# Performance work log

Hardware: AMD Instinct MI355X
Metric: run time of the kernel (lower is better)

The kernel has to match this reference:

```python
import jax, jax.numpy as jnp
import numpy as np

GOP = 4


def conv3x3(x, w, b):
    y = jax.lax.conv_general_dilated(x, w, (1, 1), 'SAME',
                                     dimension_numbers=('NCHW', 'OIHW', 'NCHW'))
    return y + b[None, :, None, None]


def resize_bilinear(x, oh, ow):
    # F.interpolate(mode='bilinear', align_corners=False), no antialias
    N, C, H, W = x.shape
    ys = (jnp.arange(oh, dtype=x.dtype) + 0.5) * (H / oh) - 0.5
    xs = (jnp.arange(ow, dtype=x.dtype) + 0.5) * (W / ow) - 0.5
    y0 = jnp.floor(ys); x0 = jnp.floor(xs)
    ty = (ys - y0)[:, None]; tx = (xs - x0)[None, :]
    y0i = jnp.clip(y0, 0, H - 1).astype(jnp.int32)
    y1i = jnp.clip(y0 + 1, 0, H - 1).astype(jnp.int32)
    x0i = jnp.clip(x0, 0, W - 1).astype(jnp.int32)
    x1i = jnp.clip(x0 + 1, 0, W - 1).astype(jnp.int32)
    r00 = x[:, :, y0i][:, :, :, x0i]; r01 = x[:, :, y0i][:, :, :, x1i]
    r10 = x[:, :, y1i][:, :, :, x0i]; r11 = x[:, :, y1i][:, :, :, x1i]
    top = r00 * (1 - tx) + r01 * tx
    bot = r10 * (1 - tx) + r11 * tx
    return top * (1 - ty) + bot * ty


def deform_sample_1x1(feat, off):
    # torchvision deform_conv2d with 1x1 kernel: bilinear gather at
    # (h + dy, w + dx), zero outside; offset channels are (dy, dx).
    N, C, H, W = feat.shape
    dy, dx = off[:, 0], off[:, 1]                       # [N,H,W]
    gy = jnp.arange(H, dtype=feat.dtype)[:, None] + dy  # [N,H,W]
    gx = jnp.arange(W, dtype=feat.dtype)[None, :] + dx
    y0 = jnp.floor(gy); x0 = jnp.floor(gx)
    ty = (gy - y0)[:, None]; tx = (gx - x0)[:, None]    # [N,1,H,W]

    def corner(yi, xi):
        valid = (yi >= 0) & (yi < H) & (xi >= 0) & (xi < W)
        yc = jnp.clip(yi, 0, H - 1).astype(jnp.int32)
        xc = jnp.clip(xi, 0, W - 1).astype(jnp.int32)
        v = jax.vmap(lambda f, y, x: f[:, y, x])(feat, yc, xc)  # [N,C,H,W]
        return v * valid[:, None].astype(feat.dtype)

    return (corner(y0, x0) * (1 - ty) * (1 - tx)
            + corner(y0, x0 + 1) * (1 - ty) * tx
            + corner(y0 + 1, x0) * ty * (1 - tx)
            + corner(y0 + 1, x0 + 1) * ty * tx)


def setup_inputs() -> dict:
    key = jax.random.key(0)
    ks = jax.random.split(key, 20)
    dim = 256
    f32 = jnp.float32

    def p(k, shape, s=0.05):
        return jax.random.normal(k, shape, dtype=f32) * s

    return {
        'imgs': jax.random.normal(ks[0], (2, 16, 3, 224, 224), dtype=f32),
        'i_features': jax.random.normal(ks[1], (8, dim, 56, 56), dtype=f32),
        'p_motions': jax.random.normal(ks[2], (2, 12, 2, 112, 112), dtype=f32),
        'dw': p(ks[3], (dim, dim)), 'db': p(ks[4], (dim,)),
        'mw1': p(ks[5], (dim, dim, 3, 3)), 'mb1': p(ks[6], (dim,)),
        'mw2': p(ks[7], (dim, dim, 3, 3)), 'mb2': p(ks[8], (dim,)),
        'mw3': p(ks[9], (dim, dim, 3, 3)), 'mb3': p(ks[10], (dim,)),
        'ew1': p(ks[11], (dim, 2, 3, 3)), 'eb1': p(ks[12], (dim,)),
        'ew2': p(ks[13], (dim, dim, 3, 3)), 'eb2': p(ks[14], (dim,)),
        'ew3': p(ks[15], (dim, dim, 3, 3)), 'eb3': p(ks[16], (dim,)),
        'ew4': p(ks[17], (dim, dim, 3, 3)), 'eb4': p(ks[18], (dim,)),
    }


def reference(imgs, i_features, p_motions, dw, db, mw1, mb1, mw2, mb2, mw3, mb3,
              ew1, eb1, ew2, eb2, ew3, eb3, ew4, eb4):
    B = imgs.shape[0]
    num_gop = imgs.shape[1] // GOP
    h, w = i_features.shape[-2], i_features.shape[-1]
    scale = h / imgs.shape[-1]  # static python float
    Tp = p_motions.shape[1]
    k = Tp // num_gop

    # flatten motions over (b t), resize to feature res, rescale magnitudes
    pm = p_motions.reshape(B * Tp, 2, p_motions.shape[-2], p_motions.shape[-1])
    pm = resize_bilinear(pm, h, w) * scale              # [(b n k), 2, h, w]

    emb = jax.nn.relu(conv3x3(pm, ew1, eb1))
    emb = jax.nn.relu(conv3x3(emb, ew2, eb2))
    emb = jax.nn.relu(conv3x3(emb, ew3, eb3))
    emb = jax.nn.relu(conv3x3(emb, ew4, eb4))

    # i_features expanded to one copy per P-frame: (b n) -> (b n k)
    feat = jnp.repeat(i_features, k, axis=0)
    sampled = deform_sample_1x1(feat, pm)
    pf = jnp.einsum('nchw,oc->nohw', sampled, dw) + db[None, :, None, None]

    pf = jax.nn.relu(conv3x3(pf, mw1, mb1))
    pf = jax.nn.relu(conv3x3(pf, mw2, mb2))
    pf = jax.nn.relu(conv3x3(pf, mw3, mb3))
    p2d = pf + emb                                      # [(b n k), c, h, w]

    # adaptive_avg_pool2d(1) + flatten(3)
    pooled = p2d.reshape(B, num_gop, k, -1, h, w).mean(axis=(-2, -1))  # [b,n,k,c]
    return pooled, p2d
```

## Files before the change

### kernel.cpp

```cpp
#include <hip/hip_runtime.h>

#define NPIX 3136
#define NN   24
#define CDIM 256

typedef __attribute__((ext_vector_type(8))) short short8v;
typedef __attribute__((ext_vector_type(4))) float float4v;

typedef __attribute__((address_space(1))) const void gvoid;
typedef __attribute__((address_space(3))) void lvoid;
static __device__ __forceinline__ void async_copy16(const void* g, void* l) {
    __builtin_amdgcn_global_load_lds((gvoid*)g, (lvoid*)l, 16, 0, 0);
}

static __device__ __forceinline__ unsigned short f2b(float f) {
    unsigned int u = __float_as_uint(f);
    u = (u + 0x7FFFu + ((u >> 16) & 1u)) >> 16;
    return (unsigned short)u;
}
static __device__ __forceinline__ float b2f(unsigned short h) {
    return __uint_as_float(((unsigned int)h) << 16);
}

__global__ __launch_bounds__(256) void resize_pm_kernel(
    const float* __restrict__ pmo, float* __restrict__ pm)
{
    int idx = blockIdx.x * 256 + threadIdx.x;
    if (idx >= NN * 2 * NPIX) return;
    int x = idx % 56, y = (idx / 56) % 56, nc = idx / NPIX;
    const float* src = pmo + (size_t)nc * 112 * 112 + (size_t)(2 * y) * 112 + 2 * x;
    pm[idx] = (src[0] + src[1] + src[112] + src[113]) * 0.0625f;
}

__global__ __launch_bounds__(256) void pack_all_kernel(
    const float* __restrict__ s0, const float* __restrict__ s1,
    const float* __restrict__ s2, const float* __restrict__ s3,
    const float* __restrict__ s4, const float* __restrict__ s5,
    const float* __restrict__ sdw, unsigned short* __restrict__ dstbase)
{
    int bx = blockIdx.x;
    if (bx < 6 * 2304) {
        int wi = bx / 2304;
        int d = (bx % 2304) * 256 + threadIdx.x;
        const float* w = (wi == 0) ? s0 : (wi == 1) ? s1 : (wi == 2) ? s2
                       : (wi == 3) ? s3 : (wi == 4) ? s4 : s5;
        int j = d & 7;
        int lane = (d >> 3) & 63;
        int g = (d >> 9) & 3;
        int e = d >> 11;
        int tap = e % 9;
        int f = e / 9;
        int ch = f & 7, cb = f >> 3;
        int co = cb * 64 + g * 16 + (lane & 15);
        int ci = ch * 32 + (lane >> 4) * 8 + j;
        dstbase[(size_t)wi * 589824 + d] = f2b(w[((size_t)co * 256 + ci) * 9 + tap]);
    } else {
        int d = (bx - 6 * 2304) * 256 + threadIdx.x;
        int j = d & 7;
        int lane = (d >> 3) & 63;
        int g = (d >> 9) & 3;
        int ch = (d >> 11) & 7;
        int cb = d >> 14;
        int co = cb * 64 + g * 16 + (lane & 15);
        int ci = ch * 32 + (lane >> 4) * 8 + j;
        dstbase[(size_t)6 * 589824 + d] = f2b(sdw[(size_t)co * 256 + ci]);
    }
}

__global__ __launch_bounds__(256) void ew1_kernel(
    const float* __restrict__ pm, const float* __restrict__ w,
    const float* __restrict__ b, unsigned short* __restrict__ out)
{
    __shared__ float sT[8][18];
    __shared__ float sW1[256 * 19];
    int n = blockIdx.y;
    int pixbase = blockIdx.x * 8;
    int t = threadIdx.x;
    if (t < 144) {
        int p = t / 18, j = t % 18;
        int ci = j / 9, tap = j % 9;
        int pix = pixbase + p;
        int y = pix / 56, x = pix % 56;
        int yy = y + tap / 3 - 1, xx = x + tap % 3 - 1;
        float v = 0.f;
        if ((unsigned)yy < 56u && (unsigned)xx < 56u)
            v = pm[((size_t)n * 2 + ci) * NPIX + yy * 56 + xx];
        sT[p][j] = v;
    }
    for (int idx = t; idx < 4608; idx += 256) {
        int co = idx / 18, j = idx % 18;
        sW1[co * 19 + j] = w[idx];
    }
    __syncthreads();
    int co = t;
    float bias = b[co];
#pragma unroll
    for (int p = 0; p < 8; p++) {
        float acc = bias;
#pragma unroll
        for (int j = 0; j < 18; j++) acc += sT[p][j] * sW1[co * 19 + j];
        acc = fmaxf(acc, 0.f);
        out[((size_t)n * NPIX + pixbase + p) * 256 + co] = f2b(acc);
    }
}

template <int TAPS, bool RELU, bool HASB, bool FUSE>
__global__ __launch_bounds__(256, 2) void conv_mfma(
    const unsigned short* __restrict__ in,
    const unsigned short* __restrict__ wp,
    const float* __restrict__ bias,
    unsigned short* __restrict__ out,
    const unsigned short* __restrict__ emb,
    float* __restrict__ dout)
{
    constexpr int W_ITERS = TAPS * 4;
    constexpr int SIN_SHORTS = (TAPS == 9) ? 10 * 58 * 32 : 448 * 32;

    __shared__ unsigned short sIn[SIN_SHORTS];
    __shared__ unsigned short sW[W_ITERS * 512];

    const int r0 = blockIdx.x * 8;
    if (r0 >= 56) return;
    const int tid = threadIdx.x;
    const int lane = tid & 63;
    const int wv = tid >> 6;
    const int col = lane & 15;
    const int quad = lane >> 4;
    const int cb = blockIdx.y;
    const int n = blockIdx.z;

    const unsigned short* inN = in + (size_t)n * NPIX * 256;
    const unsigned short* wcb = wp + (size_t)cb * 8 * W_ITERS * 512;

    int rowoff[7];
#pragma unroll
    for (int nj = 0; nj < 7; nj++) {
        int pxl = wv * 112 + nj * 16 + col;
        if (TAPS == 9) {
            int yl = pxl / 56;
            rowoff[nj] = yl * 58 + (pxl - yl * 56);
        } else {
            rowoff[nj] = pxl;
        }
    }
    const int qoff = quad * 8;
    const int laneSrc = (lane >> 2) * 256 + (lane & 3) * 8;

    if (TAPS == 9) {
        for (int i = tid * 8; i < SIN_SHORTS; i += 2048)
            *(int4*)(sIn + i) = (int4){0, 0, 0, 0};
    }

    float4v acc[4][7];
#pragma unroll
    for (int mi = 0; mi < 4; mi++)
#pragma unroll
        for (int nj = 0; nj < 7; nj++) acc[mi][nj] = (float4v){0.f, 0.f, 0.f, 0.f};

    for (int ch = 0; ch < 8; ch++) {
        const int c0 = ch * 32;
        __syncthreads();
        const unsigned short* wchunk = wcb + (size_t)ch * W_ITERS * 512;
#pragma unroll
        for (int it = wv; it < W_ITERS; it += 4)
            async_copy16(wchunk + it * 512 + lane * 8, sW + it * 512);
        if (TAPS == 9) {
#pragma unroll
            for (int ry = 0; ry < 10; ry++) {
                int k = (wv - ry) & 3;
                int gy = r0 + ry - 1;
                if ((unsigned)gy < 56u && (k < 3 || lane < 32))
                    async_copy16(inN + (size_t)gy * 14336 + k * 4096 + c0 + laneSrc,
                                 sIn + ry * 1856 + 32 + k * 512);
            }
        } else {
#pragma unroll
            for (int k = 0; k < 7; k++) {
                int it = wv + k * 4;
                async_copy16(inN + (size_t)r0 * 14336 + it * 4096 + c0 + laneSrc,
                             sIn + it * 512);
            }
        }
        __syncthreads();
#pragma unroll
        for (int tap = 0; tap < TAPS; tap++) {
            const int coff = (TAPS == 9) ? ((tap / 3) * 58 + (tap % 3)) * 32 : 0;
            short8v a[4], b[7];
#pragma unroll
            for (int mi = 0; mi < 4; mi++)
                a[mi] = *(const short8v*)(sW + ((tap * 4 + mi) * 64 + lane) * 8);
#pragma unroll
            for (int nj = 0; nj < 7; nj++)
                b[nj] = *(const short8v*)(sIn + rowoff[nj] * 32 + coff + qoff);
#pragma unroll
            for (int mi = 0; mi < 4; mi++)
#pragma unroll
                for (int nj = 0; nj < 7; nj++)
                    acc[mi][nj] = __builtin_amdgcn_mfma_f32_16x16x32_bf16(
                        a[mi], b[nj], acc[mi][nj], 0, 0, 0);
        }
    }

    if (!FUSE) {
        unsigned short* outT = out + ((size_t)n * NPIX + r0 * 56 + wv * 112) * 256 + cb * 64;
#pragma unroll
        for (int mi = 0; mi < 4; mi++) {
            float4v bv = (float4v){0.f, 0.f, 0.f, 0.f};
            if (HASB) bv = *(const float4v*)(bias + cb * 64 + mi * 16 + quad * 4);
#pragma unroll
            for (int nj = 0; nj < 7; nj++) {
                float v0 = acc[mi][nj][0] + bv[0];
                float v1 = acc[mi][nj][1] + bv[1];
                float v2 = acc[mi][nj][2] + bv[2];
                float v3 = acc[mi][nj][3] + bv[3];
                if (RELU) {
                    v0 = fmaxf(v0, 0.f); v1 = fmaxf(v1, 0.f);
                    v2 = fmaxf(v2, 0.f); v3 = fmaxf(v3, 0.f);
                }
                uint2 pk;
                pk.x = (unsigned)f2b(v0) | ((unsigned)f2b(v1) << 16);
                pk.y = (unsigned)f2b(v2) | ((unsigned)f2b(v3) << 16);
                *(uint2*)(outT + ((size_t)(nj * 16 + col)) * 256 + mi * 16 + quad * 4) = pk;
            }
        }
    } else {
        const int pixBase = r0 * 56 + wv * 112;
        float* p2d = dout + 6144 + (size_t)n * CDIM * NPIX;
        float sums[4][4];
#pragma unroll
        for (int mi = 0; mi < 4; mi++)
#pragma unroll
            for (int q = 0; q < 4; q++) sums[mi][q] = 0.f;
#pragma unroll
        for (int mi = 0; mi < 4; mi++) {
            float4v bv = *(const float4v*)(bias + cb * 64 + mi * 16 + quad * 4);
            const int co0 = cb * 64 + mi * 16 + quad * 4;
#pragma unroll
            for (int nj = 0; nj < 7; nj++) {
                int pix = pixBase + nj * 16 + col;
                uint2 e = *(const uint2*)(emb + ((size_t)n * NPIX + pix) * 256 + co0);
                float v0 = fmaxf(acc[mi][nj][0] + bv[0], 0.f) + b2f((unsigned short)(e.x & 0xFFFF));
                float v1 = fmaxf(acc[mi][nj][1] + bv[1], 0.f) + b2f((unsigned short)(e.x >> 16));
                float v2 = fmaxf(acc[mi][nj][2] + bv[2], 0.f) + b2f((unsigned short)(e.y & 0xFFFF));
                float v3 = fmaxf(acc[mi][nj][3] + bv[3], 0.f) + b2f((unsigned short)(e.y >> 16));
                p2d[(size_t)(co0 + 0) * NPIX + pix] = v0;
                p2d[(size_t)(co0 + 1) * NPIX + pix] = v1;
                p2d[(size_t)(co0 + 2) * NPIX + pix] = v2;
                p2d[(size_t)(co0 + 3) * NPIX + pix] = v3;
                sums[mi][0] += v0; sums[mi][1] += v1;
                sums[mi][2] += v2; sums[mi][3] += v3;
            }
        }
#pragma unroll
        for (int mi = 0; mi < 4; mi++)
#pragma unroll
            for (int q = 0; q < 4; q++) {
                float s = sums[mi][q];
                s += __shfl_down(s, 8, 16);
                s += __shfl_down(s, 4, 16);
                s += __shfl_down(s, 2, 16);
                s += __shfl_down(s, 1, 16);
                if (col == 0)
                    atomicAdd(dout + n * CDIM + cb * 64 + mi * 16 + quad * 4 + q,
                              s * (1.f / 3136.f));
            }
    }
}

__global__ __launch_bounds__(256) void transpose_fI(
    const float* __restrict__ feat, unsigned short* __restrict__ dst)
{
    __shared__ float s[64][65];
    int fi = blockIdx.z;
    int p0 = blockIdx.x * 64;
    int c0 = blockIdx.y * 64;
    int t = threadIdx.x;
    int pl = t & 63, cq = t >> 6;
#pragma unroll
    for (int i = 0; i < 16; i++) {
        int c = cq + i * 4;
        s[pl][c] = feat[((size_t)fi * 256 + c0 + c) * NPIX + p0 + pl];
    }
    __syncthreads();
    int cl = t & 63, pq = t >> 6;
#pragma unroll
    for (int i = 0; i < 16; i++) {
        int p = pq + i * 4;
        dst[((size_t)fi * NPIX + p0 + p) * 256 + c0 + cl] = f2b(s[p][cl]);
    }
}

__global__ __launch_bounds__(256) void deform_kernel(
    const unsigned short* __restrict__ Z,
    const float* __restrict__ pm,
    const float* __restrict__ db,
    unsigned short* __restrict__ out)
{
    int n = blockIdx.y;
    int t = threadIdx.x;
    int pix = blockIdx.x * 8 + (t >> 5);
    int g = t & 31;
    int fi = n / 3;
    int y = pix / 56, x = pix % 56;
    float dy = pm[((size_t)n * 2 + 0) * NPIX + pix];
    float dx = pm[((size_t)n * 2 + 1) * NPIX + pix];
    float gy = (float)y + dy, gx = (float)x + dx;
    float y0f = floorf(gy), x0f = floorf(gx);
    float ty = gy - y0f, tx = gx - x0f;
    int y0 = (int)y0f, x0 = (int)x0f, y1 = y0 + 1, x1 = x0 + 1;
    bool vy0 = (unsigned)y0 < 56u, vy1 = (unsigned)y1 < 56u;
    bool vx0 = (unsigned)x0 < 56u, vx1 = (unsigned)x1 < 56u;
    float w00 = (1.f - ty) * (1.f - tx) * (vy0 && vx0 ? 1.f : 0.f);
    float w01 = (1.f - ty) * tx * (vy0 && vx1 ? 1.f : 0.f);
    float w10 = ty * (1.f - tx) * (vy1 && vx0 ? 1.f : 0.f);
    float w11 = ty * tx * (vy1 && vx1 ? 1.f : 0.f);
    int y0c = vy0 ? y0 : 0, y1c = vy1 ? y1 : 0;
    int x0c = vx0 ? x0 : 0, x1c = vx1 ? x1 : 0;
    const unsigned short* Zf = Z + (size_t)fi * NPIX * 256 + g * 8;
    const unsigned short* p00 = Zf + (size_t)(y0c * 56 + x0c) * 256;
    const unsigned short* p01 = Zf + (size_t)(y0c * 56 + x1c) * 256;
    const unsigned short* p10 = Zf + (size_t)(y1c * 56 + x0c) * 256;
    const unsigned short* p11 = Zf + (size_t)(y1c * 56 + x1c) * 256;
    unsigned short r[8];
#pragma unroll
    for (int j = 0; j < 8; j++) {
        float v = b2f(p00[j]) * w00 + b2f(p01[j]) * w01 +
                  b2f(p10[j]) * w10 + b2f(p11[j]) * w11;
        v += db[g * 8 + j];
        r[j] = f2b(v);
    }
    *(int4*)(out + ((size_t)n * NPIX + pix) * 256 + g * 8) = *(int4*)r;
}

extern "C" void kernel_launch(void* const* d_in, const int* in_sizes, int n_in,
                              void* d_out, int out_size, void* d_ws, size_t ws_size,
                              hipStream_t stream)
{
    const float* i_features = (const float*)d_in[1];
    const float* p_motions  = (const float*)d_in[2];
    const float* dw  = (const float*)d_in[3];
    const float* db  = (const float*)d_in[4];
    const float* mw1 = (const float*)d_in[5];
    const float* mb1 = (const float*)d_in[6];
    const float* mw2 = (const float*)d_in[7];
    const float* mb2 = (const float*)d_in[8];
    const float* mw3 = (const float*)d_in[9];
    const float* mb3 = (const float*)d_in[10];
    const float* ew1 = (const float*)d_in[11];
    const float* eb1 = (const float*)d_in[12];
    const float* ew2 = (const float*)d_in[13];
    const float* eb2 = (const float*)d_in[14];
    const float* ew3 = (const float*)d_in[15];
    const float* eb3 = (const float*)d_in[16];
    const float* ew4 = (const float*)d_in[17];
    const float* eb4 = (const float*)d_in[18];
    float* out = (float*)d_out;

    char* p = (char*)d_ws;
    float* pm = (float*)p;            p += 602112;
    unsigned short* wpk = (unsigned short*)p;
    unsigned short* wpE2 = wpk + 0 * 589824;
    unsigned short* wpE3 = wpk + 1 * 589824;
    unsigned short* wpE4 = wpk + 2 * 589824;
    unsigned short* wpM1 = wpk + 3 * 589824;
    unsigned short* wpM2 = wpk + 4 * 589824;
    unsigned short* wpM3 = wpk + 5 * 589824;
    unsigned short* wpDW = wpk + 6 * 589824;
    p += (6 * 589824 + 65536) * 2;
    unsigned short* actA = (unsigned short*)p; p += 38535168;
    unsigned short* actB = (unsigned short*)p; p += 38535168;
    unsigned short* embB = (unsigned short*)p; p += 38535168;

    hipMemsetAsync(out, 0, 6144 * sizeof(float), stream);

    resize_pm_kernel<<<(NN * 2 * NPIX + 255) / 256, 256, 0, stream>>>(p_motions, pm);
    pack_all_kernel<<<6 * 2304 + 256, 256, 0, stream>>>(
        ew2, ew3, ew4, mw1, mw2, mw3, dw, wpk);

    ew1_kernel<<<dim3(392, NN), 256, 0, stream>>>(pm, ew1, eb1, actA);
    dim3 cg24(8, 4, NN), cg8(8, 4, 8);
    conv_mfma<9, true, true, false><<<cg24, 256, 0, stream>>>(actA, wpE2, eb2, actB, nullptr, nullptr);
    conv_mfma<9, true, true, false><<<cg24, 256, 0, stream>>>(actB, wpE3, eb3, actA, nullptr, nullptr);
    conv_mfma<9, true, true, false><<<cg24, 256, 0, stream>>>(actA, wpE4, eb4, embB, nullptr, nullptr);

    transpose_fI<<<dim3(49, 4, 8), 256, 0, stream>>>(i_features, actA);
    conv_mfma<1, false, false, false><<<cg8, 256, 0, stream>>>(actA, wpDW, nullptr, actB, nullptr, nullptr);
    deform_kernel<<<dim3(392, NN), 256, 0, stream>>>(actB, pm, db, actA);

    conv_mfma<9, true, true, false><<<cg24, 256, 0, stream>>>(actA, wpM1, mb1, actB, nullptr, nullptr);
    conv_mfma<9, true, true, false><<<cg24, 256, 0, stream>>>(actB, wpM2, mb2, actA, nullptr, nullptr);
    conv_mfma<9, true, true, true><<<cg24, 256, 0, stream>>>(actA, wpM3, mb3, nullptr, embB, out);
}
```

Measured before the change: 712.1 us.

## Co-launch independent embedding and motion conv layers in one paired grid

Adds a second set of input, weight, bias and output pointers plus a z-split to the MFMA conv kernel. Blocks past the split run the other branch's layer. Embedding convs 3 and 4 now run in the same launch as motion convs 1 and 2, doubling the grid. The aim is to cut wave-quantization tail and launch count on this small per-layer grid. It needs a fourth activation buffer and falls back to the old sequential schedule when the workspace is too small.

```diff
diff --git a/kernel.cpp b/kernel.cpp
--- a/kernel.cpp
+++ b/kernel.cpp
@@ -110,6 +110,11 @@
     const unsigned short* __restrict__ wp,
     const float* __restrict__ bias,
     unsigned short* __restrict__ out,
+    const unsigned short* __restrict__ inB,
+    const unsigned short* __restrict__ wpB,
+    const float* __restrict__ biasB,
+    unsigned short* __restrict__ outB,
+    int zsplit,
     const unsigned short* __restrict__ emb,
     float* __restrict__ dout)
 {
@@ -127,10 +132,19 @@
     const int col = lane & 15;
     const int quad = lane >> 4;
     const int cb = blockIdx.y;
-    const int n = blockIdx.z;
-
-    const unsigned short* inN = in + (size_t)n * NPIX * 256;
-    const unsigned short* wcb = wp + (size_t)cb * 8 * W_ITERS * 512;
+
+    int n = blockIdx.z;
+    const unsigned short* inP = in;
+    const unsigned short* wpP = wp;
+    const float* biasP = bias;
+    unsigned short* outP = out;
+    if (n >= zsplit) {
+        n -= zsplit;
+        inP = inB; wpP = wpB; biasP = biasB; outP = outB;
+    }
+
+    const unsigned short* inN = inP + (size_t)n * NPIX * 256;
+    const unsigned short* wcb = wpP + (size_t)cb * 8 * W_ITERS * 512;
 
     int rowoff[7];
 #pragma unroll
@@ -202,11 +216,11 @@
     }
 
     if (!FUSE) {
-        unsigned short* outT = out + ((size_t)n * NPIX + r0 * 56 + wv * 112) * 256 + cb * 64;
+        unsigned short* outT = outP + ((size_t)n * NPIX + r0 * 56 + wv * 112) * 256 + cb * 64;
 #pragma unroll
         for (int mi = 0; mi < 4; mi++) {
             float4v bv = (float4v){0.f, 0.f, 0.f, 0.f};
-            if (HASB) bv = *(const float4v*)(bias + cb * 64 + mi * 16 + quad * 4);
+            if (HASB) bv = *(const float4v*)(biasP + cb * 64 + mi * 16 + quad * 4);
 #pragma unroll
             for (int nj = 0; nj < 7; nj++) {
                 float v0 = acc[mi][nj][0] + bv[0];
@@ -233,7 +247,7 @@
             for (int q = 0; q < 4; q++) sums[mi][q] = 0.f;
 #pragma unroll
         for (int mi = 0; mi < 4; mi++) {
-            float4v bv = *(const float4v*)(bias + cb * 64 + mi * 16 + quad * 4);
+            float4v bv = *(const float4v*)(biasP + cb * 64 + mi * 16 + quad * 4);
             const int co0 = cb * 64 + mi * 16 + quad * 4;
 #pragma unroll
             for (int nj = 0; nj < 7; nj++) {
@@ -356,8 +370,11 @@
     const float* eb4 = (const float*)d_in[18];
     float* out = (float*)d_out;
 
+    const size_t SZ_PM  = 602112;
+    const size_t SZ_WPK = 7208960;
+    const size_t SZ_ACT = 38535168;
     char* p = (char*)d_ws;
-    float* pm = (float*)p;            p += 602112;
+    float* pm = (float*)p;            p += SZ_PM;
     unsigned short* wpk = (unsigned short*)p;
     unsigned short* wpE2 = wpk + 0 * 589824;
     unsigned short* wpE3 = wpk + 1 * 589824;
@@ -366,10 +383,13 @@
     unsigned short* wpM2 = wpk + 4 * 589824;
     unsigned short* wpM3 = wpk + 5 * 589824;
     unsigned short* wpDW = wpk + 6 * 589824;
-    p += (6 * 589824 + 65536) * 2;
-    unsigned short* actA = (unsigned short*)p; p += 38535168;
-    unsigned short* actB = (unsigned short*)p; p += 38535168;
-    unsigned short* embB = (unsigned short*)p; p += 38535168;
+    p += SZ_WPK;
+    unsigned short* bufA = (unsigned short*)p; p += SZ_ACT;
+    unsigned short* bufB = (unsigned short*)p; p += SZ_ACT;
+    unsigned short* bufC = (unsigned short*)p; p += SZ_ACT;
+    unsigned short* bufD = (unsigned short*)p;
+
+    const bool paired = ws_size >= SZ_PM + SZ_WPK + 4 * SZ_ACT;
 
     hipMemsetAsync(out, 0, 6144 * sizeof(float), stream);
 
@@ -377,17 +397,41 @@
     pack_all_kernel<<<6 * 2304 + 256, 256, 0, stream>>>(
         ew2, ew3, ew4, mw1, mw2, mw3, dw, wpk);
 
-    ew1_kernel<<<dim3(392, NN), 256, 0, stream>>>(pm, ew1, eb1, actA);
-    dim3 cg24(8, 4, NN), cg8(8, 4, 8);
-    conv_mfma<9, true, true, false><<<cg24, 256, 0, stream>>>(actA, wpE2, eb2, actB, nullptr, nullptr);
-    conv_mfma<9, true, true, false><<<cg24, 256, 0, stream>>>(actB, wpE3, eb3, actA, nullptr, nullptr);
-    conv_mfma<9, true, true, false><<<cg24, 256, 0, stream>>>(actA, wpE4, eb4, embB, nullptr, nullptr);
-
-    transpose_fI<<<dim3(49, 4, 8), 256, 0, stream>>>(i_features, actA);
-    conv_mfma<1, false, false, false><<<cg8, 256, 0, stream>>>(actA, wpDW, nullptr, actB, nullptr, nullptr);
-    deform_kernel<<<dim3(392, NN), 256, 0, stream>>>(actB, pm, db, actA);
-
-    conv_mfma<9, true, true, false><<<cg24, 256, 0, stream>>>(actA, wpM1, mb1, actB, nullptr, nullptr);
-    conv_mfma<9, true, true, false><<<cg24, 256, 0, stream>>>(actB, wpM2, mb2, actA, nullptr, nullptr);
-    conv_mfma<9, true, true, true><<<cg24, 256, 0, stream>>>(actA, wpM3, mb3, nullptr, embB, out);
-}
+    dim3 cg24(8, 4, NN), cg48(8, 4, 2 * NN), cg8(8, 4, 8);
+
+    if (paired) {
+        ew1_kernel<<<dim3(392, NN), 256, 0, stream>>>(pm, ew1, eb1, bufA);
+        conv_mfma<9, true, true, false><<<cg24, 256, 0, stream>>>(
+            bufA, wpE2, eb2, bufB,  bufA, wpE2, eb2, bufB, NN, nullptr, nullptr);
+        unsigned short* fI = bufA;
+        unsigned short* Zb = bufA + (size_t)8 * NPIX * 256;
+        transpose_fI<<<dim3(49, 4, 8), 256, 0, stream>>>(i_features, fI);
+        conv_mfma<1, false, false, false><<<cg8, 256, 0, stream>>>(
+            fI, wpDW, nullptr, Zb,  fI, wpDW, nullptr, Zb, NN, nullptr, nullptr);
+        deform_kernel<<<dim3(392, NN), 256, 0, stream>>>(Zb, pm, db, bufC);
+        conv_mfma<9, true, true, false><<<cg48, 256, 0, stream>>>(
+            bufB, wpE3, eb3, bufA,  bufC, wpM1, mb1, bufD, NN, nullptr, nullptr);
+        conv_mfma<9, true, true, false><<<cg48, 256, 0, stream>>>(
+            bufA, wpE4, eb4, bufB,  bufD, wpM2, mb2, bufC, NN, nullptr, nullptr);
+        conv_mfma<9, true, true, true><<<cg24, 256, 0, stream>>>(
+            bufC, wpM3, mb3, nullptr,  bufC, wpM3, mb3, nullptr, NN, bufB, out);
+    } else {
+        ew1_kernel<<<dim3(392, NN), 256, 0, stream>>>(pm, ew1, eb1, bufA);
+        conv_mfma<9, true, true, false><<<cg24, 256, 0, stream>>>(
+            bufA, wpE2, eb2, bufB,  bufA, wpE2, eb2, bufB, NN, nullptr, nullptr);
+        conv_mfma<9, true, true, false><<<cg24, 256, 0, stream>>>(
+            bufB, wpE3, eb3, bufA,  bufB, wpE3, eb3, bufA, NN, nullptr, nullptr);
+        conv_mfma<9, true, true, false><<<cg24, 256, 0, stream>>>(
+            bufA, wpE4, eb4, bufC,  bufA, wpE4, eb4, bufC, NN, nullptr, nullptr);
+        transpose_fI<<<dim3(49, 4, 8), 256, 0, stream>>>(i_features, bufA);
+        conv_mfma<1, false, false, false><<<cg8, 256, 0, stream>>>(
+            bufA, wpDW, nullptr, bufB,  bufA, wpDW, nullptr, bufB, NN, nullptr, nullptr);
+        deform_kernel<<<dim3(392, NN), 256, 0, stream>>>(bufB, pm, db, bufA);
+        conv_mfma<9, true, true, false><<<cg24, 256, 0, stream>>>(
+            bufA, wpM1, mb1, bufB,  bufA, wpM1, mb1, bufB, NN, nullptr, nullptr);
+        conv_mfma<9, true, true, false><<<cg24, 256, 0, stream>>>(
+            bufB, wpM2, mb2, bufA,  bufB, wpM2, mb2, bufA, NN, nullptr, nullptr);
+        conv_mfma<9, true, true, true><<<cg24, 256, 0, stream>>>(
+            bufA, wpM3, mb3, nullptr,  bufA, wpM3, mb3, nullptr, NN, bufC, out);
+    }
+}
```

Result: faster. 692.3 us (-2.8%).
